# Performance work log

Measured on AMD Instinct MI355X. Metric: run time of the kernel, lower is better.

Reference implementation:

```python
import jax, jax.numpy as jnp
import numpy as np

N_PATCH, N_Z, K, BS = 16, 128, 10, 1024
D = N_PATCH * N_Z


def setup_inputs() -> dict:
    key = jax.random.key(0)
    k1, k2, k3, k4 = jax.random.split(key, 4)
    z = jax.random.normal(k1, (BS, D), dtype=jnp.float32)
    m = jax.random.normal(k2, (K, D), dtype=jnp.float32)
    L = jax.random.normal(k3, (K, D, D), dtype=jnp.float32)
    components = jax.random.randint(k4, (BS,), 0, K, dtype=jnp.int64)
    return {"z": z, "m": m, "L": L, "components": components}


def reference(z, m, L, components):
    # samps[k] = m[k] + z @ L[k].T   -> (K, BS, D)
    samps = jnp.einsum('bd,ked->kbe', z, L) + m[:, None, :]
    # one-hot mask-and-sum over components == gather selected expert per sample
    x = samps[components, jnp.arange(z.shape[0])]  # (BS, D)
    return x.reshape(-1, N_PATCH, N_Z)
```

## Files before the change

### kernel.cpp

```cpp
#include <hip/hip_runtime.h>
#include <hip/hip_bf16.h>


#define DDIM  2048
#define BSAMP 1024
#define KCOMP 10
#define MPAD  160

typedef __attribute__((ext_vector_type(8))) short bf16x8;
typedef __attribute__((ext_vector_type(4))) float f32x4;

__device__ __forceinline__ short bfs(float x) {
    __hip_bfloat16 h = __float2bfloat16(x);
    return *reinterpret_cast<short*>(&h);
}

__global__ void build_map(const int* __restrict__ comp,
                          int* __restrict__ rowmap,
                          int* __restrict__ counts) {
    __shared__ int sc[KCOMP];
    const int t = threadIdx.x;
    if (t < KCOMP) sc[t] = 0;
    __syncthreads();
    const int c = comp[t];
    const int r = atomicAdd(&sc[c], 1);
    if (r < MPAD) rowmap[c * MPAD + r] = t;
    __syncthreads();
    if (t < KCOMP) counts[t] = sc[t];
}

__global__ void zprep(const float* __restrict__ z,
                      const int* __restrict__ rowmap,
                      short* __restrict__ zfrag) {
    const int idx  = blockIdx.x * 256 + threadIdx.x;
    const int lane = idx & 63;
    const int rest = idx >> 6;
    const int ms   = rest % 10;
    const int kit  = rest / 10;
    const int it   = kit & 63;
    const int k    = kit >> 6;
    const int slot = ms * 16 + (lane & 15);
    const int r    = rowmap[k * MPAD + slot] & (BSAMP - 1);
    const int d    = it * 32 + (lane >> 4) * 8;
    const float* zp = z + (size_t)r * DDIM + d;
    f32x4 a = *(const f32x4*)zp;
    f32x4 b = *(const f32x4*)(zp + 4);
    bf16x8 o;
#pragma unroll
    for (int j = 0; j < 4; ++j) { o[j] = bfs(a[j]); o[4 + j] = bfs(b[j]); }
    *(bf16x8*)(zfrag + (size_t)idx * 8) = o;
}

template <int MT>
__device__ __forceinline__ void gmm_body(
        const short* __restrict__ Ab,
        const float* __restrict__ Bp,
        const float* __restrict__ mvec,
        const int* __restrict__ rowmap,
        float* __restrict__ out,
        int k, int mh, int e, int cnt, int lane) {
    f32x4 acc[MT];
#pragma unroll
    for (int mt = 0; mt < MT; ++mt) acc[mt] = (f32x4){0.f, 0.f, 0.f, 0.f};

#pragma unroll 2
    for (int it = 0; it < DDIM / 32; ++it) {
        f32x4 bx = *(const f32x4*)(Bp);
        f32x4 by = *(const f32x4*)(Bp + 4);
        bf16x8 b;
#pragma unroll
        for (int j = 0; j < 4; ++j) { b[j] = bfs(bx[j]); b[4 + j] = bfs(by[j]); }
#pragma unroll
        for (int mt = 0; mt < MT; ++mt) {
            bf16x8 a = *(const bf16x8*)(Ab + mt * 512);
            acc[mt] = __builtin_amdgcn_mfma_f32_16x16x32_bf16(a, b, acc[mt], 0, 0, 0);
        }
        Ab += 5120;
        Bp += 32;
    }

    const float mu  = mvec[k * DDIM + e];
    const int rquad = (lane >> 4) * 4;
    const int rmB   = k * MPAD;
#pragma unroll
    for (int mt = 0; mt < MT; ++mt) {
        const int sb = mh * 80 + mt * 16 + rquad;
#pragma unroll
        for (int r = 0; r < 4; ++r) {
            const int slot = sb + r;
            if (slot < cnt) {
                const int bidx = rowmap[rmB + slot];
                out[(size_t)bidx * DDIM + e] = acc[mt][r] + mu;
            }
        }
    }
}

__global__ __launch_bounds__(128, 4)
void gmm_direct(const short* __restrict__ zfrag,
                const float* __restrict__ mvec,
                const float* __restrict__ Lmat,
                const int* __restrict__ rowmap,
                const int* __restrict__ counts,
                float* __restrict__ out) {
    const int t = threadIdx.x, lane = t & 63, nh = t >> 6;
    const int n  = blockIdx.x;
    const int k  = blockIdx.y;
    const int mh = blockIdx.z;
    const int cnt = counts[k];
    const int rem = cnt - mh * 80;
    if (rem <= 0) return;
    const int nmt = (rem >= 80) ? 5 : ((rem + 15) >> 4);

    const int e = n * 32 + nh * 16 + (lane & 15);
    const short* Ab = zfrag + ((size_t)(k * 64) * 10 + mh * 5) * 512 + lane * 8;
    const float* Bp = Lmat + (size_t)k * DDIM * DDIM + (size_t)e * DDIM
                    + (lane >> 4) * 8;

    switch (nmt) {
        case 5: gmm_body<5>(Ab, Bp, mvec, rowmap, out, k, mh, e, cnt, lane); break;
        case 4: gmm_body<4>(Ab, Bp, mvec, rowmap, out, k, mh, e, cnt, lane); break;
        case 3: gmm_body<3>(Ab, Bp, mvec, rowmap, out, k, mh, e, cnt, lane); break;
        case 2: gmm_body<2>(Ab, Bp, mvec, rowmap, out, k, mh, e, cnt, lane); break;
        default: gmm_body<1>(Ab, Bp, mvec, rowmap, out, k, mh, e, cnt, lane); break;
    }
}

typedef bf16x8 bf8_t;
__device__ __forceinline__ void async16(void* lds, const void* g) {
    __builtin_amdgcn_global_load_lds(
        (const __attribute__((address_space(1))) void*)g,
        (__attribute__((address_space(3))) void*)lds, 16, 0, 0);
}
__device__ __forceinline__ bf16x8 frag8(const char* base, int o0, int o1) {
    f32x4 x = *(const f32x4*)(base + o0);
    f32x4 y = *(const f32x4*)(base + o1);
    bf16x8 r;
#pragma unroll
    for (int i = 0; i < 4; ++i) { r[i] = bfs(x[i]); r[4 + i] = bfs(y[i]); }
    return r;
}
__global__ __launch_bounds__(256, 2)
void gmm_f32z(const float* __restrict__ z, const float* __restrict__ mvec,
              const float* __restrict__ Lmat, const int* __restrict__ rowmap,
              const int* __restrict__ counts, float* __restrict__ out) {
    __shared__ __attribute__((aligned(16))) char smem[2 * 28672];
    const int t = threadIdx.x, lane = t & 63, w = t >> 6;
    const int mh = w >> 1, nh = w & 1;
    const int k = blockIdx.y, n0 = blockIdx.x * 64;
    const float* Lk = Lmat + (size_t)k * DDIM * DDIM;
    const int rq = t >> 3;
    const int scol = ((t & 7) ^ (rq & 7)) * 4;
    int rm[5];
#pragma unroll
    for (int j = 0; j < 5; ++j)
        rm[j] = rowmap[k * MPAD + j * 32 + rq] & (BSAMP - 1);
    const unsigned ub = (unsigned)(t & ~63) * 16;
    auto stage = [&](int buf, int it) {
        char* lb = smem + buf * 28672;
        const int d0 = it * 32 + scol;
#pragma unroll
        for (int j = 0; j < 5; ++j)
            async16(lb + j * 4096 + ub, z + (size_t)rm[j] * DDIM + d0);
        async16(lb + 20480 + ub,        Lk + (size_t)(n0 + rq) * DDIM + d0);
        async16(lb + 20480 + 4096 + ub, Lk + (size_t)(n0 + 32 + rq) * DDIM + d0);
    };
    f32x4 acc[5][2];
#pragma unroll
    for (int mt = 0; mt < 5; ++mt)
#pragma unroll
        for (int nt = 0; nt < 2; ++nt) acc[mt][nt] = (f32x4){0.f, 0.f, 0.f, 0.f};
    stage(0, 0);
    __syncthreads();
    const int fr = lane & 15, g0 = (lane >> 4) * 2;
    for (int it = 0; it < DDIM / 32; ++it) {
        if (it + 1 < DDIM / 32) stage((it + 1) & 1, it + 1);
        const char* lb = smem + (it & 1) * 28672;
        const int rb0 = nh * 32 + fr, rb1 = rb0 + 16;
        bf16x8 b0 = frag8(lb + 20480, rb0 * 128 + ((g0 ^ rb0) & 7) * 16,
                          rb0 * 128 + (((g0 + 1) ^ rb0) & 7) * 16);
        bf16x8 b1 = frag8(lb + 20480, rb1 * 128 + ((g0 ^ rb1) & 7) * 16,
                          rb1 * 128 + (((g0 + 1) ^ rb1) & 7) * 16);
#pragma unroll
        for (int mt = 0; mt < 5; ++mt) {
            const int ra = mh * 80 + mt * 16 + fr;
            bf16x8 a = frag8(lb, ra * 128 + ((g0 ^ ra) & 7) * 16,
                             ra * 128 + (((g0 + 1) ^ ra) & 7) * 16);
            acc[mt][0] = __builtin_amdgcn_mfma_f32_16x16x32_bf16(a, b0, acc[mt][0], 0, 0, 0);
            acc[mt][1] = __builtin_amdgcn_mfma_f32_16x16x32_bf16(a, b1, acc[mt][1], 0, 0, 0);
        }
        __syncthreads();
    }
    const int cnt = counts[k], rquad = (lane >> 4) * 4;
#pragma unroll
    for (int nt = 0; nt < 2; ++nt) {
        const int e = n0 + nh * 32 + nt * 16 + fr;
        const float mu = mvec[k * DDIM + e];
#pragma unroll
        for (int mt = 0; mt < 5; ++mt) {
            const int sb = mh * 80 + mt * 16 + rquad;
#pragma unroll
            for (int r = 0; r < 4; ++r) {
                const int slot = sb + r;
                if (slot < cnt)
                    out[(size_t)rowmap[k * MPAD + slot] * DDIM + e] = acc[mt][nt][r] + mu;
            }
        }
    }
}

extern "C" void kernel_launch(void* const* d_in, const int* in_sizes, int n_in,
                              void* d_out, int out_size, void* d_ws, size_t ws_size,
                              hipStream_t stream) {
    const float* z    = (const float*)d_in[0];
    const float* mvec = (const float*)d_in[1];
    const float* Lmat = (const float*)d_in[2];
    const int* comp   = (const int*)d_in[3];
    float* out        = (float*)d_out;

    int* rowmap = (int*)d_ws;
    int* counts = rowmap + KCOMP * MPAD;
    build_map<<<1, BSAMP, 0, stream>>>(comp, rowmap, counts);

    const size_t zf_off = 8192;
    const size_t zf_sz  = (size_t)KCOMP * 64 * 10 * 64 * 16;

    if (ws_size >= zf_off + zf_sz) {
        short* zfrag = (short*)((char*)d_ws + zf_off);
        zprep<<<1600, 256, 0, stream>>>(z, rowmap, zfrag);
        gmm_direct<<<dim3(64, KCOMP, 2), 128, 0, stream>>>(
            zfrag, mvec, Lmat, rowmap, counts, out);
    } else {
        gmm_f32z<<<dim3(32, KCOMP), 256, 0, stream>>>(
            z, mvec, Lmat, rowmap, counts, out);
    }
}
```

Before: 287.0 us.

## Software-pipeline L loads 8 deep and interleave mh halves in grid

```diff
diff --git a/kernel.cpp b/kernel.cpp
--- a/kernel.cpp
+++ b/kernel.cpp
@@ -53,7 +53,7 @@
 
 template <int MT>
 __device__ __forceinline__ void gmm_body(
-        const short* __restrict__ Ab,
+        const short* __restrict__ Ap,
         const float* __restrict__ Bp,
         const float* __restrict__ mvec,
         const int* __restrict__ rowmap,
@@ -63,20 +63,42 @@
 #pragma unroll
     for (int mt = 0; mt < MT; ++mt) acc[mt] = (f32x4){0.f, 0.f, 0.f, 0.f};
 
-#pragma unroll 2
-    for (int it = 0; it < DDIM / 32; ++it) {
-        f32x4 bx = *(const f32x4*)(Bp);
-        f32x4 by = *(const f32x4*)(Bp + 4);
+    f32x4 Bw[8][2];
+    bf16x8 A0[MT], A1[MT];
+#pragma unroll
+    for (int j = 0; j < 8; ++j) {
+        Bw[j][0] = *(const f32x4*)(Bp + j * 32);
+        Bw[j][1] = *(const f32x4*)(Bp + j * 32 + 4);
+    }
+#pragma unroll
+    for (int mt = 0; mt < MT; ++mt) A0[mt] = *(const bf16x8*)(Ap + mt * 512);
+
+    const float* Bpf = Bp + 8 * 32;
+    const short* Apf = Ap + 5120;
+    int it = 0;
+
+    auto step = [&](bf16x8* Ac, bf16x8* An, f32x4* Bs) {
+#pragma unroll
+        for (int mt = 0; mt < MT; ++mt) An[mt] = *(const bf16x8*)(Apf + mt * 512);
+        f32x4 nb0 = *(const f32x4*)(Bpf);
+        f32x4 nb1 = *(const f32x4*)(Bpf + 4);
         bf16x8 b;
 #pragma unroll
-        for (int j = 0; j < 4; ++j) { b[j] = bfs(bx[j]); b[4 + j] = bfs(by[j]); }
-#pragma unroll
-        for (int mt = 0; mt < MT; ++mt) {
-            bf16x8 a = *(const bf16x8*)(Ab + mt * 512);
-            acc[mt] = __builtin_amdgcn_mfma_f32_16x16x32_bf16(a, b, acc[mt], 0, 0, 0);
-        }
-        Ab += 5120;
-        Bp += 32;
+        for (int j = 0; j < 4; ++j) { b[j] = bfs(Bs[0][j]); b[4 + j] = bfs(Bs[1][j]); }
+#pragma unroll
+        for (int mt = 0; mt < MT; ++mt)
+            acc[mt] = __builtin_amdgcn_mfma_f32_16x16x32_bf16(Ac[mt], b, acc[mt], 0, 0, 0);
+        Bs[0] = nb0; Bs[1] = nb1;
+        ++it;
+        if (it < 63) Apf += 5120;
+        if (it < 56) Bpf += 32;
+    };
+
+    for (int ot = 0; ot < 8; ++ot) {
+        step(A0, A1, Bw[0]); step(A1, A0, Bw[1]);
+        step(A0, A1, Bw[2]); step(A1, A0, Bw[3]);
+        step(A0, A1, Bw[4]); step(A1, A0, Bw[5]);
+        step(A0, A1, Bw[6]); step(A1, A0, Bw[7]);
     }
 
     const float mu  = mvec[k * DDIM + e];
@@ -96,7 +118,7 @@
     }
 }
 
-__global__ __launch_bounds__(128, 4)
+__global__ __launch_bounds__(128, 2)
 void gmm_direct(const short* __restrict__ zfrag,
                 const float* __restrict__ mvec,
                 const float* __restrict__ Lmat,
@@ -104,29 +126,28 @@
                 const int* __restrict__ counts,
                 float* __restrict__ out) {
     const int t = threadIdx.x, lane = t & 63, nh = t >> 6;
-    const int n  = blockIdx.x;
+    const int n  = blockIdx.x >> 1;
+    const int mh = blockIdx.x & 1;
     const int k  = blockIdx.y;
-    const int mh = blockIdx.z;
     const int cnt = counts[k];
     const int rem = cnt - mh * 80;
     if (rem <= 0) return;
     const int nmt = (rem >= 80) ? 5 : ((rem + 15) >> 4);
 
     const int e = n * 32 + nh * 16 + (lane & 15);
-    const short* Ab = zfrag + ((size_t)(k * 64) * 10 + mh * 5) * 512 + lane * 8;
+    const short* Ap = zfrag + ((size_t)(k * 64) * 10 + mh * 5) * 512 + lane * 8;
     const float* Bp = Lmat + (size_t)k * DDIM * DDIM + (size_t)e * DDIM
                     + (lane >> 4) * 8;
 
     switch (nmt) {
-        case 5: gmm_body<5>(Ab, Bp, mvec, rowmap, out, k, mh, e, cnt, lane); break;
-        case 4: gmm_body<4>(Ab, Bp, mvec, rowmap, out, k, mh, e, cnt, lane); break;
-        case 3: gmm_body<3>(Ab, Bp, mvec, rowmap, out, k, mh, e, cnt, lane); break;
-        case 2: gmm_body<2>(Ab, Bp, mvec, rowmap, out, k, mh, e, cnt, lane); break;
-        default: gmm_body<1>(Ab, Bp, mvec, rowmap, out, k, mh, e, cnt, lane); break;
-    }
-}
-
-typedef bf16x8 bf8_t;
+        case 5: gmm_body<5>(Ap, Bp, mvec, rowmap, out, k, mh, e, cnt, lane); break;
+        case 4: gmm_body<4>(Ap, Bp, mvec, rowmap, out, k, mh, e, cnt, lane); break;
+        case 3: gmm_body<3>(Ap, Bp, mvec, rowmap, out, k, mh, e, cnt, lane); break;
+        case 2: gmm_body<2>(Ap, Bp, mvec, rowmap, out, k, mh, e, cnt, lane); break;
+        default: gmm_body<1>(Ap, Bp, mvec, rowmap, out, k, mh, e, cnt, lane); break;
+    }
+}
+
 __device__ __forceinline__ void async16(void* lds, const void* g) {
     __builtin_amdgcn_global_load_lds(
         (const __attribute__((address_space(1))) void*)g,
@@ -228,7 +249,7 @@
     if (ws_size >= zf_off + zf_sz) {
         short* zfrag = (short*)((char*)d_ws + zf_off);
         zprep<<<1600, 256, 0, stream>>>(z, rowmap, zfrag);
-        gmm_direct<<<dim3(64, KCOMP, 2), 128, 0, stream>>>(
+        gmm_direct<<<dim3(128, KCOMP), 128, 0, stream>>>(
             zfrag, mvec, Lmat, rowmap, counts, out);
     } else {
         gmm_f32z<<<dim3(32, KCOMP), 256, 0, stream>>>(
```

New measurement: 279.8 us. -2.5%, faster.
